# Performance work log

Measured on AMD Instinct MI355X. Metric: run time of the kernel, lower is better.

## Reference

```python
import jax, jax.numpy as jnp
import numpy as np

N = 50000
E = 800000
F_IN = 500
H = 5          # heads
C = 32         # per-head channels
HID = H * C    # 160
NC = 20        # num_classes
G = 8          # number of graphs in batch
SLOPE_ATT = 0.2   # GATConv attention leaky slope (PyG default)
SLOPE_ACT = 0.01  # F.leaky_relu default


def _layernorm(x, scale, bias, eps=1e-5):
    mu = jnp.mean(x, axis=-1, keepdims=True)
    var = jnp.var(x, axis=-1, keepdims=True)
    return (x - mu) * jax.lax.rsqrt(var + eps) * scale + bias


def _edge_softmax(logits, dst, num_nodes):
    # segment softmax over incoming edges of each destination node
    m = jax.ops.segment_max(logits, dst, num_segments=num_nodes)
    ex = jnp.exp(logits - m[dst])
    s = jax.ops.segment_sum(ex, dst, num_segments=num_nodes)
    return ex / (s[dst] + 1e-16)


def _gat_layer(x, src, dst, W, a_src, a_dst, b):
    n = x.shape[0]
    h = (x @ W).reshape(n, H, C)                       # [N,H,C]
    al_s = jnp.einsum('nhc,hc->nh', h, a_src)          # [N,H]
    al_d = jnp.einsum('nhc,hc->nh', h, a_dst)
    logits = jax.nn.leaky_relu(al_s[src] + al_d[dst], SLOPE_ATT)  # [Et,H]
    alpha = _edge_softmax(logits, dst, n)              # [Et,H]
    msg = h[src] * alpha[..., None]                    # [Et,H,C]
    out = jax.ops.segment_sum(msg, dst, num_segments=n).reshape(n, HID) + b
    return out, alpha


def setup_inputs():
    key = jax.random.key(0)
    ks = jax.random.split(key, 24)
    p = lambda k, shp: jax.random.normal(k, shp, jnp.float32) * 0.05
    x = jax.random.normal(ks[0], (N, F_IN), jnp.float32)
    edge_index = jax.random.randint(ks[1], (2, E), 0, N, jnp.int64)
    batch = jnp.sort(jax.random.randint(ks[2], (N,), 0, G, jnp.int64))
    return {
        'x': x, 'edge_index': edge_index, 'batch': batch,
        'W1': p(ks[3], (F_IN, HID)), 'a_src1': p(ks[4], (H, C)), 'a_dst1': p(ks[5], (H, C)), 'b1': jnp.zeros((HID,), jnp.float32),
        'ln1_s': jnp.ones((HID,), jnp.float32), 'ln1_b': jnp.zeros((HID,), jnp.float32),
        'W2': p(ks[6], (HID, HID)), 'a_src2': p(ks[7], (H, C)), 'a_dst2': p(ks[8], (H, C)), 'b2': jnp.zeros((HID,), jnp.float32),
        'ln2_s': jnp.ones((HID,), jnp.float32), 'ln2_b': jnp.zeros((HID,), jnp.float32),
        'Wm': p(ks[9], (HID, HID)), 'bm': jnp.zeros((HID,), jnp.float32),
        'Wmlp1': p(ks[10], (HID, HID)), 'bmlp1': jnp.zeros((HID,), jnp.float32),
        'ln3_s': jnp.ones((HID,), jnp.float32), 'ln3_b': jnp.zeros((HID,), jnp.float32),
        'Wmlp2': p(ks[11], (HID, NC)), 'bmlp2': jnp.zeros((NC,), jnp.float32),
    }


def reference(x, edge_index, batch, W1, a_src1, a_dst1, b1, ln1_s, ln1_b,
              W2, a_src2, a_dst2, b2, ln2_s, ln2_b, Wm, bm,
              Wmlp1, bmlp1, ln3_s, ln3_b, Wmlp2, bmlp2):
    n = x.shape[0]
    # PyG GATConv adds self-loops by default
    loops = jnp.arange(n, dtype=edge_index.dtype)
    src = jnp.concatenate([edge_index[0], loops])
    dst = jnp.concatenate([edge_index[1], loops])

    h1, alpha1 = _gat_layer(x, src, dst, W1, a_src1, a_dst1, b1)
    h1 = jax.nn.leaky_relu(h1, SLOPE_ACT)
    h1 = _layernorm(h1, ln1_s, ln1_b)      # dropout = identity at eval

    h2, alpha2 = _gat_layer(h1, src, dst, W2, a_src2, a_dst2, b2)
    h2 = jax.nn.leaky_relu(h2, SLOPE_ACT)
    h2 = _layernorm(h2, ln2_s, ln2_b)

    xo = jax.nn.leaky_relu(h2 @ Wm + bm, SLOPE_ACT)   # [N,HID]

    # global_mean_pool over batch assignment
    sums = jax.ops.segment_sum(xo, batch, num_segments=G)
    cnts = jax.ops.segment_sum(jnp.ones((n, 1), xo.dtype), batch, num_segments=G)
    pooled = sums / jnp.maximum(cnts, 1.0)            # [G,HID]

    z = pooled @ Wmlp1 + bmlp1
    z = jax.nn.relu(_layernorm(z, ln3_s, ln3_b))
    rec = z @ Wmlp2 + bmlp2                           # [G,NC]
    return xo, rec, alpha1, alpha2
```

## Files before the change

kernel.cpp:

```cpp
#include <hip/hip_runtime.h>
#include <hip/hip_bf16.h>
#include <cstdint>
#include <cstddef>

#define NN   50000
#define EE   800000
#define ET_  (EE + NN)
#define FIN  500
#define HID_ 160
#define NC_  20
#define GG   8

typedef __attribute__((ext_vector_type(8))) short ab8;
typedef __attribute__((ext_vector_type(4))) float f4;

static __device__ __forceinline__ unsigned short f2bf(float v) {
    union { float f; uint32_t u; } c; c.f = v;
    uint32_t r = c.u + 0x7FFFu + ((c.u >> 16) & 1u);
    return (unsigned short)(r >> 16);
}

static __device__ __forceinline__ float2 bf2f2(uint32_t u) {
    union { uint32_t u; float f; } a, b;
    a.u = u << 16;
    b.u = u & 0xffff0000u;
    return make_float2(a.f, b.f);
}

static __device__ __forceinline__ int lbound_i(const int* arr, int n, int val) {
    int lo = 0, hi = n;
    while (lo < hi) { int mid = (lo + hi) >> 1; if (arr[mid] < val) lo = mid + 1; else hi = mid; }
    return lo;
}

__global__ __launch_bounds__(256) void k_hist(const int* __restrict__ ei, int* __restrict__ deg) {
    int e = blockIdx.x * 256 + threadIdx.x;
    if (e >= ET_) return;
    int d = (e < EE) ? ei[EE + e] : (e - EE);
    atomicAdd(&deg[d], 1);
}

__global__ __launch_bounds__(256) void k_scan1(const int* __restrict__ deg, int* __restrict__ rowptr,
                                               int* __restrict__ bsum) {
    __shared__ int s[256];
    int t = threadIdx.x;
    int base = blockIdx.x * 1024 + t * 4;
    int v0 = (base + 0 < NN) ? deg[base + 0] : 0;
    int v1 = (base + 1 < NN) ? deg[base + 1] : 0;
    int v2 = (base + 2 < NN) ? deg[base + 2] : 0;
    int v3 = (base + 3 < NN) ? deg[base + 3] : 0;
    int tot = v0 + v1 + v2 + v3;
    s[t] = tot;
    __syncthreads();
    for (int off = 1; off < 256; off <<= 1) {
        int y = (t >= off) ? s[t - off] : 0;
        __syncthreads();
        s[t] += y;
        __syncthreads();
    }
    int excl = s[t] - tot;
    if (t == 255) bsum[blockIdx.x] = s[255];
    if (base + 0 < NN) rowptr[base + 0] = excl;  excl += v0;
    if (base + 1 < NN) rowptr[base + 1] = excl;  excl += v1;
    if (base + 2 < NN) rowptr[base + 2] = excl;  excl += v2;
    if (base + 3 < NN) rowptr[base + 3] = excl;
}

__global__ void k_scan2(int* __restrict__ bsum, int nb) {
    int t = threadIdx.x;
    int v = (t < nb) ? bsum[t] : 0;
    int orig = v;
    for (int off = 1; off < 64; off <<= 1) {
        int y = __shfl_up(v, off);
        if (t >= off) v += y;
    }
    if (t < nb) bsum[t] = v - orig;
}

__global__ __launch_bounds__(256) void k_scan3(int* __restrict__ rowptr, const int* __restrict__ bsum,
                                               int* __restrict__ cursor) {
    int i = blockIdx.x * 256 + threadIdx.x;
    if (i < NN) {
        int r = rowptr[i] + bsum[i >> 10];
        rowptr[i] = r;
        cursor[i] = r;
    }
    if (i == NN) rowptr[NN] = ET_;
}

__global__ __launch_bounds__(256) void k_scatter(const int* __restrict__ ei, int* __restrict__ cursor,
                                                 int2* __restrict__ epair) {
    int e = blockIdx.x * 256 + threadIdx.x;
    if (e >= ET_) return;
    int s, d;
    if (e < EE) { s = ei[e]; d = ei[EE + e]; } else { s = e - EE; d = e - EE; }
    int slot = atomicAdd(&cursor[d], 1);
    epair[slot] = make_int2(e, s);
}

__global__ __launch_bounds__(256) void k_prep_all(const float* __restrict__ W1, unsigned short* __restrict__ Wt1,
                                                  const float* __restrict__ W2, unsigned short* __restrict__ Wt2,
                                                  const float* __restrict__ Wm, unsigned short* __restrict__ Wmt) {
    int idx = blockIdx.x * 256 + threadIdx.x;
    const int S1 = HID_ * 512, S2 = HID_ * HID_;
    if (idx < S1) {
        int n = idx / 512, k = idx - n * 512;
        Wt1[idx] = (k < FIN) ? f2bf(W1[(size_t)k * HID_ + n]) : (unsigned short)0;
    } else if (idx < S1 + S2) {
        int j = idx - S1;
        int n = j / HID_, k = j - n * HID_;
        Wt2[j] = f2bf(W2[(size_t)k * HID_ + n]);
    } else if (idx < S1 + 2 * S2) {
        int j = idx - S1 - S2;
        int n = j / HID_, k = j - n * HID_;
        Wmt[j] = f2bf(Wm[(size_t)k * HID_ + n]);
    }
}

__global__ __launch_bounds__(256) void k_gemm_mfma(const void* __restrict__ Av,
                                                   const unsigned short* __restrict__ Bt,
                                                   float* __restrict__ C, __hip_bfloat16* __restrict__ Cb,
                                                   int M, int K, int Kp, int a_bf16,
                                                   const float* __restrict__ bias, int act,
                                                   const float* __restrict__ asrc, const float* __restrict__ adst,
                                                   float* __restrict__ als_o, float* __restrict__ ald_o,
                                                   const int* __restrict__ batch_p, float* __restrict__ pooled) {
    __shared__ __align__(16) unsigned short As[128 * 40];
    __shared__ __align__(16) unsigned short Bs[160 * 40];
    int tid  = threadIdx.x;
    int lane = tid & 63;
    int w    = tid >> 6;
    int fr   = lane & 15;
    int q8   = (lane >> 4) * 8;
    int row0 = blockIdx.x * 128;

    int arow  = tid >> 1;
    int abase = (tid & 1) * 16;

    f4 acc0[10], acc1[10];
#pragma unroll
    for (int t = 0; t < 10; t++) { acc0[t] = (f4)0.f; acc1[t] = (f4)0.f; }

    for (int k0 = 0; k0 < Kp; k0 += 32) {
        {
            int grow = row0 + arow;
            int bk = k0 + abase;
            if (a_bf16) {
                const unsigned short* Ab = (const unsigned short*)Av;
                ab8 v0 = (ab8)0, v1 = (ab8)0;
                if (grow < M) {
                    v0 = *reinterpret_cast<const ab8*>(&Ab[(size_t)grow * K + bk]);
                    v1 = *reinterpret_cast<const ab8*>(&Ab[(size_t)grow * K + bk + 8]);
                }
                *reinterpret_cast<ab8*>(&As[arow * 40 + abase])     = v0;
                *reinterpret_cast<ab8*>(&As[arow * 40 + abase + 8]) = v1;
            } else {
                const float* A = (const float*)Av;
                unsigned short pk[16];
                if (grow < M && bk + 16 <= K) {
                    const float4* src = reinterpret_cast<const float4*>(&A[(size_t)grow * K + bk]);
#pragma unroll
                    for (int f = 0; f < 4; f++) {
                        float4 v = src[f];
                        pk[f * 4 + 0] = f2bf(v.x); pk[f * 4 + 1] = f2bf(v.y);
                        pk[f * 4 + 2] = f2bf(v.z); pk[f * 4 + 3] = f2bf(v.w);
                    }
                } else {
#pragma unroll
                    for (int c = 0; c < 16; c++) {
                        int k = bk + c;
                        pk[c] = (grow < M && k < K) ? f2bf(A[(size_t)grow * K + k]) : (unsigned short)0;
                    }
                }
                *reinterpret_cast<ab8*>(&As[arow * 40 + abase])     = *reinterpret_cast<ab8*>(&pk[0]);
                *reinterpret_cast<ab8*>(&As[arow * 40 + abase + 8]) = *reinterpret_cast<ab8*>(&pk[8]);
            }
        }
        {
            for (int idx = tid; idx < 640; idx += 256) {
                int n = idx >> 2, c4 = (idx & 3) * 8;
                ab8 v = *reinterpret_cast<const ab8*>(&Bt[(size_t)n * Kp + k0 + c4]);
                *reinterpret_cast<ab8*>(&Bs[n * 40 + c4]) = v;
            }
        }
        __syncthreads();
        ab8 a0 = *reinterpret_cast<const ab8*>(&As[(w * 16 + fr) * 40 + q8]);
        ab8 a1 = *reinterpret_cast<const ab8*>(&As[(w * 16 + 64 + fr) * 40 + q8]);
#pragma unroll
        for (int t = 0; t < 10; t++) {
            ab8 b = *reinterpret_cast<const ab8*>(&Bs[(t * 16 + fr) * 40 + q8]);
            acc0[t] = __builtin_amdgcn_mfma_f32_16x16x32_bf16(a0, b, acc0[t], 0, 0, 0);
            acc1[t] = __builtin_amdgcn_mfma_f32_16x16x32_bf16(a1, b, acc1[t], 0, 0, 0);
        }
        __syncthreads();
    }

    int q = lane >> 4;
    if (als_o) {
        float av_s[10], av_d[10];
#pragma unroll
        for (int t = 0; t < 10; t++) { av_s[t] = asrc[t * 16 + fr]; av_d[t] = adst[t * 16 + fr]; }
#pragma unroll
        for (int s = 0; s < 2; s++) {
            const f4* ac = s ? acc1 : acc0;
#pragma unroll
            for (int i = 0; i < 4; i++) {
                int r = row0 + w * 16 + q * 4 + i + s * 64;
                float ps[5], pd[5];
#pragma unroll
                for (int h = 0; h < 5; h++) {
                    ps[h] = ac[2 * h][i] * av_s[2 * h] + ac[2 * h + 1][i] * av_s[2 * h + 1];
                    pd[h] = ac[2 * h][i] * av_d[2 * h] + ac[2 * h + 1][i] * av_d[2 * h + 1];
                }
#pragma unroll
                for (int off = 8; off >= 1; off >>= 1)
#pragma unroll
                    for (int h = 0; h < 5; h++) {
                        ps[h] += __shfl_xor(ps[h], off);
                        pd[h] += __shfl_xor(pd[h], off);
                    }
                if (fr == 0 && r < M) {
#pragma unroll
                    for (int h = 0; h < 5; h++) {
                        als_o[(size_t)r * 5 + h] = ps[h];
                        ald_o[(size_t)r * 5 + h] = pd[h];
                    }
                }
            }
        }
    }

    int gu = -2;
    if (pooled) {
        int gl = batch_p[row0];
        int rhi = row0 + 127; if (rhi >= M) rhi = M - 1;
        int gh = batch_p[rhi];
        gu = (gl == gh) ? gl : -1;
    }
    float psum[10];
#pragma unroll
    for (int t = 0; t < 10; t++) psum[t] = 0.f;

    int rbase0 = row0 + w * 16 + q * 4;
#pragma unroll
    for (int t = 0; t < 10; t++) {
        int col = t * 16 + fr;
        float bv = bias ? bias[col] : 0.f;
#pragma unroll
        for (int i = 0; i < 4; i++) {
            int r0 = rbase0 + i;
            int r1 = r0 + 64;
            float v0 = acc0[t][i] + bv;
            float v1 = acc1[t][i] + bv;
            if (act) { v0 = v0 > 0.f ? v0 : 0.01f * v0; v1 = v1 > 0.f ? v1 : 0.01f * v1; }
            if (r0 < M) {
                if (C)  C[(size_t)r0 * HID_ + col] = v0;
                if (Cb) *reinterpret_cast<unsigned short*>(&Cb[(size_t)r0 * HID_ + col]) = f2bf(v0);
            }
            if (r1 < M) {
                if (C)  C[(size_t)r1 * HID_ + col] = v1;
                if (Cb) *reinterpret_cast<unsigned short*>(&Cb[(size_t)r1 * HID_ + col]) = f2bf(v1);
            }
            if (gu >= 0) {
                if (r0 < M) psum[t] += v0;
                if (r1 < M) psum[t] += v1;
            } else if (gu == -1) {
                if (r0 < M) atomicAdd(&pooled[batch_p[r0] * HID_ + col], v0);
                if (r1 < M) atomicAdd(&pooled[batch_p[r1] * HID_ + col], v1);
            }
        }
    }
    if (gu >= 0) {
#pragma unroll
        for (int t = 0; t < 10; t++) {
            psum[t] += __shfl_xor(psum[t], 16);
            psum[t] += __shfl_xor(psum[t], 32);
        }
        if (q == 0) {
#pragma unroll
            for (int t = 0; t < 10; t++)
                atomicAdd(&pooled[gu * HID_ + t * 16 + fr], psum[t]);
        }
    }
}

__global__ __launch_bounds__(256) void k_att_agg(const int* __restrict__ rowptr,
                                                 const int2* __restrict__ epair,
                                                 const float* __restrict__ als, const float* __restrict__ ald,
                                                 const __hip_bfloat16* __restrict__ hmat,
                                                 float* __restrict__ alphap,
                                                 float* __restrict__ alpha_out,
                                                 const float* __restrict__ bias,
                                                 const float* __restrict__ lns, const float* __restrict__ lnb,
                                                 __hip_bfloat16* __restrict__ outb) {
    __shared__ float sExp[4][64 * 5];
    __shared__ int2  sPair[4][64];
    int wv   = threadIdx.x >> 6;
    int lane = threadIdx.x & 63;
    int node = blockIdx.x * 4 + wv;
    if (node >= NN) return;
    int start = rowptr[node], end = rowptr[node + 1];
    int deg = end - start;
    bool fits = (deg <= 64);
    float ad[5];
#pragma unroll
    for (int h = 0; h < 5; h++) ad[h] = ald[node * 5 + h];

    float sm[5] = {0.f, 0.f, 0.f, 0.f, 0.f};
    for (int j = start + lane; j < end; j += 64) {
        int2 p = epair[j];
        const float* as = &als[(size_t)p.y * 5];
        int idx = j - start;
        if (fits) sPair[wv][idx] = p;
#pragma unroll
        for (int h = 0; h < 5; h++) {
            float l = as[h] + ad[h];
            l = l > 0.f ? l : 0.2f * l;
            float ex = __expf(fminf(l, 60.f));
            sm[h] += ex;
            if (fits) sExp[wv][idx * 5 + h] = ex;
            else      alphap[(size_t)j * 5 + h] = ex;
        }
    }
#pragma unroll
    for (int off = 32; off >= 1; off >>= 1)
#pragma unroll
        for (int h = 0; h < 5; h++) sm[h] += __shfl_xor(sm[h], off);
    float inv[5];
#pragma unroll
    for (int h = 0; h < 5; h++) inv[h] = 1.f / (sm[h] + 1e-16f);

    int h0 = lane >> 4;
    bool lo16 = lane < 16;
    int c01 = 2 * lane;
    int c2  = 128 + 2 * lane;
    float2 A  = make_float2(0.f, 0.f), B2 = make_float2(0.f, 0.f);
    float2 A2 = make_float2(0.f, 0.f), B22 = make_float2(0.f, 0.f);

    if (fits) {
        if (lane < deg) {
            int2 p = sPair[wv][lane];
            float* ao = &alpha_out[(size_t)p.x * 5];
#pragma unroll
            for (int h = 0; h < 5; h++) ao[h] = sExp[wv][lane * 5 + h] * inv[h];
        }
        int idx = 0;
        for (; idx + 1 < deg; idx += 2) {
            int sA = sPair[wv][idx].y, sB = sPair[wv][idx + 1].y;
            float wA = sExp[wv][idx * 5 + h0] * inv[h0];
            float wB = sExp[wv][(idx + 1) * 5 + h0] * inv[h0];
            const unsigned short* rA = (const unsigned short*)&hmat[(size_t)sA * HID_];
            const unsigned short* rB = (const unsigned short*)&hmat[(size_t)sB * HID_];
            float2 fA = bf2f2(*reinterpret_cast<const uint32_t*>(&rA[c01]));
            float2 fB = bf2f2(*reinterpret_cast<const uint32_t*>(&rB[c01]));
            A.x += wA * fA.x; A.y += wA * fA.y;
            B2.x += wB * fB.x; B2.y += wB * fB.y;
            if (lo16) {
                float wA4 = sExp[wv][idx * 5 + 4] * inv[4];
                float wB4 = sExp[wv][(idx + 1) * 5 + 4] * inv[4];
                float2 gA = bf2f2(*reinterpret_cast<const uint32_t*>(&rA[c2]));
                float2 gB = bf2f2(*reinterpret_cast<const uint32_t*>(&rB[c2]));
                A2.x += wA4 * gA.x; A2.y += wA4 * gA.y;
                B22.x += wB4 * gB.x; B22.y += wB4 * gB.y;
            }
        }
        if (idx < deg) {
            int sA = sPair[wv][idx].y;
            float wA = sExp[wv][idx * 5 + h0] * inv[h0];
            const unsigned short* rA = (const unsigned short*)&hmat[(size_t)sA * HID_];
            float2 fA = bf2f2(*reinterpret_cast<const uint32_t*>(&rA[c01]));
            A.x += wA * fA.x; A.y += wA * fA.y;
            if (lo16) {
                float wA4 = sExp[wv][idx * 5 + 4] * inv[4];
                float2 gA = bf2f2(*reinterpret_cast<const uint32_t*>(&rA[c2]));
                A2.x += wA4 * gA.x; A2.y += wA4 * gA.y;
            }
        }
    } else {
        for (int j = start + lane; j < end; j += 64) {
            int2 p = epair[j];
            float* ao = &alpha_out[(size_t)p.x * 5];
#pragma unroll
            for (int h = 0; h < 5; h++) ao[h] = alphap[(size_t)j * 5 + h] * inv[h];
        }
        for (int j = start; j < end; j++) {
            int2 p = epair[j];
            const float* ap = &alphap[(size_t)j * 5];
            float wA = ap[h0] * inv[h0];
            const unsigned short* rA = (const unsigned short*)&hmat[(size_t)p.y * HID_];
            float2 fA = bf2f2(*reinterpret_cast<const uint32_t*>(&rA[c01]));
            A.x += wA * fA.x; A.y += wA * fA.y;
            if (lo16) {
                float wA4 = ap[4] * inv[4];
                float2 gA = bf2f2(*reinterpret_cast<const uint32_t*>(&rA[c2]));
                A2.x += wA4 * gA.x; A2.y += wA4 * gA.y;
            }
        }
    }
    A.x += B2.x; A.y += B2.y; A2.x += B22.x; A2.y += B22.y;

    float2 bb = *reinterpret_cast<const float2*>(&bias[c01]);
    float v0 = A.x + bb.x;  v0 = v0 > 0.f ? v0 : 0.01f * v0;
    float v1 = A.y + bb.y;  v1 = v1 > 0.f ? v1 : 0.01f * v1;
    float v2 = 0.f, v3 = 0.f;
    if (lo16) {
        float2 b2 = *reinterpret_cast<const float2*>(&bias[c2]);
        v2 = A2.x + b2.x; v2 = v2 > 0.f ? v2 : 0.01f * v2;
        v3 = A2.y + b2.y; v3 = v3 > 0.f ? v3 : 0.01f * v3;
    }
    float s  = v0 + v1 + v2 + v3;
    float sq = v0 * v0 + v1 * v1 + v2 * v2 + v3 * v3;
#pragma unroll
    for (int off = 32; off >= 1; off >>= 1) {
        s  += __shfl_xor(s, off);
        sq += __shfl_xor(sq, off);
    }
    float m = s * (1.f / 160.f);
    float r = rsqrtf(sq * (1.f / 160.f) - m * m + 1e-5f);
    size_t ob = (size_t)node * HID_;
    {
        float2 sc = *reinterpret_cast<const float2*>(&lns[c01]);
        float2 bi = *reinterpret_cast<const float2*>(&lnb[c01]);
        uint32_t pk = (uint32_t)f2bf((v0 - m) * r * sc.x + bi.x)
                    | ((uint32_t)f2bf((v1 - m) * r * sc.y + bi.y) << 16);
        *reinterpret_cast<uint32_t*>(&outb[ob + c01]) = pk;
    }
    if (lo16) {
        float2 sc = *reinterpret_cast<const float2*>(&lns[c2]);
        float2 bi = *reinterpret_cast<const float2*>(&lnb[c2]);
        uint32_t pk = (uint32_t)f2bf((v2 - m) * r * sc.x + bi.x)
                    | ((uint32_t)f2bf((v3 - m) * r * sc.y + bi.y) << 16);
        *reinterpret_cast<uint32_t*>(&outb[ob + c2]) = pk;
    }
}

__global__ __launch_bounds__(256) void k_mlp(const float* __restrict__ pooled, const int* __restrict__ batch,
                                             const float* __restrict__ W1, const float* __restrict__ b1,
                                             const float* __restrict__ lns, const float* __restrict__ lnb,
                                             const float* __restrict__ W2, const float* __restrict__ b2,
                                             float* __restrict__ rec) {
    __shared__ float P[GG][HID_];
    __shared__ float Z[GG][HID_];
    __shared__ float mu[GG], rr[GG], ic[GG];
    int t = threadIdx.x;
    if (t < GG) {
        int lo = lbound_i(batch, NN, t), hi = lbound_i(batch, NN, t + 1);
        ic[t] = 1.f / fmaxf((float)(hi - lo), 1.f);
    }
    __syncthreads();
    for (int i = t; i < GG * HID_; i += 256) P[i / HID_][i % HID_] = pooled[i] * ic[i / HID_];
    __syncthreads();
    for (int i = t; i < GG * HID_; i += 256) {
        int g = i / HID_, j = i % HID_;
        float acc = b1[j];
        for (int k = 0; k < HID_; k++) acc += P[g][k] * W1[k * HID_ + j];
        Z[g][j] = acc;
    }
    __syncthreads();
    if (t < GG) {
        float s = 0.f, sq = 0.f;
        for (int k = 0; k < HID_; k++) { float z = Z[t][k]; s += z; sq += z * z; }
        float m = s / (float)HID_;
        mu[t] = m;
        rr[t] = rsqrtf(sq / (float)HID_ - m * m + 1e-5f);
    }
    __syncthreads();
    for (int i = t; i < GG * HID_; i += 256) {
        int g = i / HID_, j = i % HID_;
        float z = (Z[g][j] - mu[g]) * rr[g] * lns[j] + lnb[j];
        Z[g][j] = fmaxf(z, 0.f);
    }
    __syncthreads();
    for (int i = t; i < GG * NC_; i += 256) {
        int g = i / NC_, j = i % NC_;
        float acc = b2[j];
        for (int k = 0; k < HID_; k++) acc += Z[g][k] * W2[k * NC_ + j];
        rec[g * NC_ + j] = acc;
    }
}

extern "C" void kernel_launch(void* const* d_in, const int* in_sizes, int n_in,
                              void* d_out, int out_size, void* d_ws, size_t ws_size,
                              hipStream_t stream) {
    const float* x    = (const float*)d_in[0];
    const int*   ei   = (const int*)d_in[1];
    const int*   batch= (const int*)d_in[2];
    const float* W1   = (const float*)d_in[3];
    const float* as1  = (const float*)d_in[4];
    const float* ad1  = (const float*)d_in[5];
    const float* b1   = (const float*)d_in[6];
    const float* ln1s = (const float*)d_in[7];
    const float* ln1b = (const float*)d_in[8];
    const float* W2   = (const float*)d_in[9];
    const float* as2  = (const float*)d_in[10];
    const float* ad2  = (const float*)d_in[11];
    const float* b2   = (const float*)d_in[12];
    const float* ln2s = (const float*)d_in[13];
    const float* ln2b = (const float*)d_in[14];
    const float* Wm   = (const float*)d_in[15];
    const float* bm   = (const float*)d_in[16];
    const float* Wm1  = (const float*)d_in[17];
    const float* bm1  = (const float*)d_in[18];
    const float* ln3s = (const float*)d_in[19];
    const float* ln3b = (const float*)d_in[20];
    const float* Wm2  = (const float*)d_in[21];
    const float* bm2  = (const float*)d_in[22];

    float* out    = (float*)d_out;
    float* xo     = out;
    float* rec    = out + (size_t)NN * HID_;
    float* alpha1 = rec + GG * NC_;
    float* alpha2 = alpha1 + (size_t)ET_ * 5;

    char* w = (char*)d_ws;
    auto carve = [&](size_t bytes) { char* p = w; w += (bytes + 255) & ~(size_t)255; return p; };
    int*   deg    = (int*)carve((size_t)NN * 4);
    int*   rowptr = (int*)carve((size_t)(NN + 1) * 4);
    int*   cursor = (int*)carve((size_t)NN * 4);
    int2*  epair  = (int2*)carve((size_t)ET_ * 8);
    int*   bsum   = (int*)carve(64 * 4);
    __hip_bfloat16* hbuf  = (__hip_bfloat16*)carve((size_t)NN * HID_ * 2);
    __hip_bfloat16* xbufb = (__hip_bfloat16*)carve((size_t)NN * HID_ * 2);
    float* alphap = (float*)carve((size_t)ET_ * 5 * 4);
    float* als    = (float*)carve((size_t)NN * 5 * 4);
    float* ald    = (float*)carve((size_t)NN * 5 * 4);
    float* pooled = (float*)carve((size_t)GG * HID_ * 4);
    unsigned short* Wt1 = (unsigned short*)carve((size_t)HID_ * 512 * 2);
    unsigned short* Wt2 = (unsigned short*)carve((size_t)HID_ * HID_ * 2);
    unsigned short* Wmt = (unsigned short*)carve((size_t)HID_ * HID_ * 2);

    hipMemsetAsync(deg, 0, (size_t)NN * 4, stream);
    k_hist<<<(ET_ + 255) / 256, 256, 0, stream>>>(ei, deg);
    int nb = (NN + 1023) / 1024;
    k_scan1<<<nb, 256, 0, stream>>>(deg, rowptr, bsum);
    k_scan2<<<1, 64, 0, stream>>>(bsum, nb);
    k_scan3<<<(NN + 1 + 255) / 256, 256, 0, stream>>>(rowptr, bsum, cursor);
    k_scatter<<<(ET_ + 255) / 256, 256, 0, stream>>>(ei, cursor, epair);

    const int PREP = HID_ * 512 + 2 * HID_ * HID_;
    k_prep_all<<<(PREP + 255) / 256, 256, 0, stream>>>(W1, Wt1, W2, Wt2, Wm, Wmt);
    hipMemsetAsync(pooled, 0, (size_t)GG * HID_ * 4, stream);

    const int NWB = (NN + 3) / 4;
    const int GB  = (NN + 127) / 128;

    k_gemm_mfma<<<GB, 256, 0, stream>>>(x, Wt1, nullptr, hbuf, NN, FIN, 512, 0, nullptr, 0,
                                        as1, ad1, als, ald, nullptr, nullptr);
    k_att_agg<<<NWB, 256, 0, stream>>>(rowptr, epair, als, ald, hbuf, alphap, alpha1,
                                       b1, ln1s, ln1b, xbufb);

    k_gemm_mfma<<<GB, 256, 0, stream>>>(xbufb, Wt2, nullptr, hbuf, NN, HID_, HID_, 1, nullptr, 0,
                                        as2, ad2, als, ald, nullptr, nullptr);
    k_att_agg<<<NWB, 256, 0, stream>>>(rowptr, epair, als, ald, hbuf, alphap, alpha2,
                                       b2, ln2s, ln2b, xbufb);

    k_gemm_mfma<<<GB, 256, 0, stream>>>(xbufb, Wmt, xo, nullptr, NN, HID_, HID_, 1, bm, 1,
                                        nullptr, nullptr, nullptr, nullptr, batch, pooled);
    k_mlp<<<1, 256, 0, stream>>>(pooled, batch, Wm1, bm1, ln3s, ln3b, Wm2, bm2, rec);
}
```

Baseline: 666.2 us.

## Rewrite GEMM to load operands straight into registers without shared memory

Measured after the change: 717.0 us. 7.6% more time.

```diff
diff --git a/kernel.cpp b/kernel.cpp
--- a/kernel.cpp
+++ b/kernel.cpp
@@ -100,9 +100,11 @@
 
 __global__ __launch_bounds__(256) void k_prep_all(const float* __restrict__ W1, unsigned short* __restrict__ Wt1,
                                                   const float* __restrict__ W2, unsigned short* __restrict__ Wt2,
-                                                  const float* __restrict__ Wm, unsigned short* __restrict__ Wmt) {
+                                                  const float* __restrict__ Wm, unsigned short* __restrict__ Wmt,
+                                                  float* __restrict__ pooled) {
     int idx = blockIdx.x * 256 + threadIdx.x;
     const int S1 = HID_ * 512, S2 = HID_ * HID_;
+    if (idx < GG * HID_) pooled[idx] = 0.f;
     if (idx < S1) {
         int n = idx / 512, k = idx - n * 512;
         Wt1[idx] = (k < FIN) ? f2bf(W1[(size_t)k * HID_ + n]) : (unsigned short)0;
@@ -117,171 +119,161 @@
     }
 }
 
-__global__ __launch_bounds__(256) void k_gemm_mfma(const void* __restrict__ Av,
+template<int ABF>
+static __device__ __forceinline__ void gemm_body(const void* __restrict__ Av,
+                                                 const unsigned short* __restrict__ Bt,
+                                                 float* __restrict__ C, __hip_bfloat16* __restrict__ Cb,
+                                                 int M, int K, int Kp,
+                                                 const float* __restrict__ bias, int act,
+                                                 const float* __restrict__ asrc, const float* __restrict__ adst,
+                                                 float* __restrict__ als_o, float* __restrict__ ald_o,
+                                                 const int* __restrict__ batch_p, float* __restrict__ pooled) {
+    int tid  = threadIdx.x;
+    int lane = tid & 63;
+    int w    = tid >> 6;
+    int fr   = lane & 15;
+    int q    = lane >> 4;
+    int row0 = blockIdx.x * 64;
+    int arow = row0 + w * 16 + fr;
+    bool rv  = arow < M;
+
+    f4 acc[10];
+#pragma unroll
+    for (int t = 0; t < 10; t++) acc[t] = (f4)0.f;
+
+    const int nk = Kp >> 5;
+    const unsigned short* bbase = Bt + (size_t)fr * Kp + q * 8;
+
+    auto loadA = [&](int s) -> ab8 {
+        ab8 a = (ab8)0;
+        int k0 = s * 32 + q * 8;
+        if (ABF) {
+            const unsigned short* Ab = (const unsigned short*)Av;
+            if (rv) a = *reinterpret_cast<const ab8*>(&Ab[(size_t)arow * K + k0]);
+        } else {
+            const float* A = (const float*)Av;
+            if (rv && k0 + 8 <= K) {
+                const float4* s4 = reinterpret_cast<const float4*>(&A[(size_t)arow * K + k0]);
+                float4 u = s4[0], v = s4[1];
+                unsigned short pk[8] = {f2bf(u.x), f2bf(u.y), f2bf(u.z), f2bf(u.w),
+                                        f2bf(v.x), f2bf(v.y), f2bf(v.z), f2bf(v.w)};
+                a = *reinterpret_cast<ab8*>(pk);
+            } else if (rv && k0 < K) {
+                unsigned short pk[8];
+#pragma unroll
+                for (int c = 0; c < 8; c++)
+                    pk[c] = (k0 + c < K) ? f2bf(A[(size_t)arow * K + k0 + c]) : (unsigned short)0;
+                a = *reinterpret_cast<ab8*>(pk);
+            }
+        }
+        return a;
+    };
+
+    ab8 acur = loadA(0);
+    for (int s = 0; s < nk; s++) {
+        ab8 anx = (ab8)0;
+        if (s + 1 < nk) anx = loadA(s + 1);
+        const unsigned short* bp = bbase + (size_t)s * 32;
+#pragma unroll
+        for (int t = 0; t < 10; t++) {
+            ab8 b = *reinterpret_cast<const ab8*>(&bp[(size_t)t * 16 * Kp]);
+            acc[t] = __builtin_amdgcn_mfma_f32_16x16x32_bf16(acur, b, acc[t], 0, 0, 0);
+        }
+        acur = anx;
+    }
+
+    if (als_o) {
+        float av_s[10], av_d[10];
+#pragma unroll
+        for (int t = 0; t < 10; t++) { av_s[t] = asrc[t * 16 + fr]; av_d[t] = adst[t * 16 + fr]; }
+#pragma unroll
+        for (int i = 0; i < 4; i++) {
+            int r = row0 + w * 16 + q * 4 + i;
+            float ps[5], pd[5];
+#pragma unroll
+            for (int h = 0; h < 5; h++) {
+                ps[h] = acc[2 * h][i] * av_s[2 * h] + acc[2 * h + 1][i] * av_s[2 * h + 1];
+                pd[h] = acc[2 * h][i] * av_d[2 * h] + acc[2 * h + 1][i] * av_d[2 * h + 1];
+            }
+#pragma unroll
+            for (int off = 8; off >= 1; off >>= 1)
+#pragma unroll
+                for (int h = 0; h < 5; h++) {
+                    ps[h] += __shfl_xor(ps[h], off);
+                    pd[h] += __shfl_xor(pd[h], off);
+                }
+            if (fr == 0 && r < M) {
+#pragma unroll
+                for (int h = 0; h < 5; h++) {
+                    als_o[(size_t)r * 5 + h] = ps[h];
+                    ald_o[(size_t)r * 5 + h] = pd[h];
+                }
+            }
+        }
+    }
+
+    int gu = -2;
+    if (pooled) {
+        int rhi = row0 + 63; if (rhi >= M) rhi = M - 1;
+        int gl = batch_p[row0], gh = batch_p[rhi];
+        gu = (gl == gh) ? gl : -1;
+    }
+    float psum[10];
+#pragma unroll
+    for (int t = 0; t < 10; t++) psum[t] = 0.f;
+
+    int rbase = row0 + w * 16 + q * 4;
+#pragma unroll
+    for (int t = 0; t < 10; t++) {
+        int col = t * 16 + fr;
+        float bv = bias ? bias[col] : 0.f;
+#pragma unroll
+        for (int i = 0; i < 4; i++) {
+            int r = rbase + i;
+            float v = acc[t][i] + bv;
+            if (act) v = v > 0.f ? v : 0.01f * v;
+            if (r < M) {
+                if (C)  C[(size_t)r * HID_ + col] = v;
+                if (Cb) *reinterpret_cast<unsigned short*>(&Cb[(size_t)r * HID_ + col]) = f2bf(v);
+                if (gu >= 0) psum[t] += v;
+                else if (gu == -1) atomicAdd(&pooled[batch_p[r] * HID_ + col], v);
+            }
+        }
+    }
+    if (gu >= 0) {
+#pragma unroll
+        for (int t = 0; t < 10; t++) {
+            psum[t] += __shfl_xor(psum[t], 16);
+            psum[t] += __shfl_xor(psum[t], 32);
+        }
+        if (q == 0) {
+#pragma unroll
+            for (int t = 0; t < 10; t++)
+                atomicAdd(&pooled[gu * HID_ + t * 16 + fr], psum[t]);
+        }
+    }
+}
+
+__global__ __launch_bounds__(256) void k_gemm_f32(const void* __restrict__ Av,
+                                                  const unsigned short* __restrict__ Bt,
+                                                  float* __restrict__ C, __hip_bfloat16* __restrict__ Cb,
+                                                  int M, int K, int Kp,
+                                                  const float* __restrict__ bias, int act,
+                                                  const float* __restrict__ asrc, const float* __restrict__ adst,
+                                                  float* __restrict__ als_o, float* __restrict__ ald_o,
+                                                  const int* __restrict__ batch_p, float* __restrict__ pooled) {
+    gemm_body<0>(Av, Bt, C, Cb, M, K, Kp, bias, act, asrc, adst, als_o, ald_o, batch_p, pooled);
+}
+
+__global__ __launch_bounds__(256) void k_gemm_bf16(const void* __restrict__ Av,
                                                    const unsigned short* __restrict__ Bt,
                                                    float* __restrict__ C, __hip_bfloat16* __restrict__ Cb,
-                                                   int M, int K, int Kp, int a_bf16,
+                                                   int M, int K, int Kp,
                                                    const float* __restrict__ bias, int act,
                                                    const float* __restrict__ asrc, const float* __restrict__ adst,
                                                    float* __restrict__ als_o, float* __restrict__ ald_o,
                                                    const int* __restrict__ batch_p, float* __restrict__ pooled) {
-    __shared__ __align__(16) unsigned short As[128 * 40];
-    __shared__ __align__(16) unsigned short Bs[160 * 40];
-    int tid  = threadIdx.x;
-    int lane = tid & 63;
-    int w    = tid >> 6;
-    int fr   = lane & 15;
-    int q8   = (lane >> 4) * 8;
-    int row0 = blockIdx.x * 128;
-
-    int arow  = tid >> 1;
-    int abase = (tid & 1) * 16;
-
-    f4 acc0[10], acc1[10];
-#pragma unroll
-    for (int t = 0; t < 10; t++) { acc0[t] = (f4)0.f; acc1[t] = (f4)0.f; }
-
-    for (int k0 = 0; k0 < Kp; k0 += 32) {
-        {
-            int grow = row0 + arow;
-            int bk = k0 + abase;
-            if (a_bf16) {
-                const unsigned short* Ab = (const unsigned short*)Av;
-                ab8 v0 = (ab8)0, v1 = (ab8)0;
-                if (grow < M) {
-                    v0 = *reinterpret_cast<const ab8*>(&Ab[(size_t)grow * K + bk]);
-                    v1 = *reinterpret_cast<const ab8*>(&Ab[(size_t)grow * K + bk + 8]);
-                }
-                *reinterpret_cast<ab8*>(&As[arow * 40 + abase])     = v0;
-                *reinterpret_cast<ab8*>(&As[arow * 40 + abase + 8]) = v1;
-            } else {
-                const float* A = (const float*)Av;
-                unsigned short pk[16];
-                if (grow < M && bk + 16 <= K) {
-                    const float4* src = reinterpret_cast<const float4*>(&A[(size_t)grow * K + bk]);
-#pragma unroll
-                    for (int f = 0; f < 4; f++) {
-                        float4 v = src[f];
-                        pk[f * 4 + 0] = f2bf(v.x); pk[f * 4 + 1] = f2bf(v.y);
-                        pk[f * 4 + 2] = f2bf(v.z); pk[f * 4 + 3] = f2bf(v.w);
-                    }
-                } else {
-#pragma unroll
-                    for (int c = 0; c < 16; c++) {
-                        int k = bk + c;
-                        pk[c] = (grow < M && k < K) ? f2bf(A[(size_t)grow * K + k]) : (unsigned short)0;
-                    }
-                }
-                *reinterpret_cast<ab8*>(&As[arow * 40 + abase])     = *reinterpret_cast<ab8*>(&pk[0]);
-                *reinterpret_cast<ab8*>(&As[arow * 40 + abase + 8]) = *reinterpret_cast<ab8*>(&pk[8]);
-            }
-        }
-        {
-            for (int idx = tid; idx < 640; idx += 256) {
-                int n = idx >> 2, c4 = (idx & 3) * 8;
-                ab8 v = *reinterpret_cast<const ab8*>(&Bt[(size_t)n * Kp + k0 + c4]);
-                *reinterpret_cast<ab8*>(&Bs[n * 40 + c4]) = v;
-            }
-        }
-        __syncthreads();
-        ab8 a0 = *reinterpret_cast<const ab8*>(&As[(w * 16 + fr) * 40 + q8]);
-        ab8 a1 = *reinterpret_cast<const ab8*>(&As[(w * 16 + 64 + fr) * 40 + q8]);
-#pragma unroll
-        for (int t = 0; t < 10; t++) {
-            ab8 b = *reinterpret_cast<const ab8*>(&Bs[(t * 16 + fr) * 40 + q8]);
-            acc0[t] = __builtin_amdgcn_mfma_f32_16x16x32_bf16(a0, b, acc0[t], 0, 0, 0);
-            acc1[t] = __builtin_amdgcn_mfma_f32_16x16x32_bf16(a1, b, acc1[t], 0, 0, 0);
-        }
-        __syncthreads();
-    }
-
-    int q = lane >> 4;
-    if (als_o) {
-        float av_s[10], av_d[10];
-#pragma unroll
-        for (int t = 0; t < 10; t++) { av_s[t] = asrc[t * 16 + fr]; av_d[t] = adst[t * 16 + fr]; }
-#pragma unroll
-        for (int s = 0; s < 2; s++) {
-            const f4* ac = s ? acc1 : acc0;
-#pragma unroll
-            for (int i = 0; i < 4; i++) {
-                int r = row0 + w * 16 + q * 4 + i + s * 64;
-                float ps[5], pd[5];
-#pragma unroll
-                for (int h = 0; h < 5; h++) {
-                    ps[h] = ac[2 * h][i] * av_s[2 * h] + ac[2 * h + 1][i] * av_s[2 * h + 1];
-                    pd[h] = ac[2 * h][i] * av_d[2 * h] + ac[2 * h + 1][i] * av_d[2 * h + 1];
-                }
-#pragma unroll
-                for (int off = 8; off >= 1; off >>= 1)
-#pragma unroll
-                    for (int h = 0; h < 5; h++) {
-                        ps[h] += __shfl_xor(ps[h], off);
-                        pd[h] += __shfl_xor(pd[h], off);
-                    }
-                if (fr == 0 && r < M) {
-#pragma unroll
-                    for (int h = 0; h < 5; h++) {
-                        als_o[(size_t)r * 5 + h] = ps[h];
-                        ald_o[(size_t)r * 5 + h] = pd[h];
-                    }
-                }
-            }
-        }
-    }
-
-    int gu = -2;
-    if (pooled) {
-        int gl = batch_p[row0];
-        int rhi = row0 + 127; if (rhi >= M) rhi = M - 1;
-        int gh = batch_p[rhi];
-        gu = (gl == gh) ? gl : -1;
-    }
-    float psum[10];
-#pragma unroll
-    for (int t = 0; t < 10; t++) psum[t] = 0.f;
-
-    int rbase0 = row0 + w * 16 + q * 4;
-#pragma unroll
-    for (int t = 0; t < 10; t++) {
-        int col = t * 16 + fr;
-        float bv = bias ? bias[col] : 0.f;
-#pragma unroll
-        for (int i = 0; i < 4; i++) {
-            int r0 = rbase0 + i;
-            int r1 = r0 + 64;
-            float v0 = acc0[t][i] + bv;
-            float v1 = acc1[t][i] + bv;
-            if (act) { v0 = v0 > 0.f ? v0 : 0.01f * v0; v1 = v1 > 0.f ? v1 : 0.01f * v1; }
-            if (r0 < M) {
-                if (C)  C[(size_t)r0 * HID_ + col] = v0;
-                if (Cb) *reinterpret_cast<unsigned short*>(&Cb[(size_t)r0 * HID_ + col]) = f2bf(v0);
-            }
-            if (r1 < M) {
-                if (C)  C[(size_t)r1 * HID_ + col] = v1;
-                if (Cb) *reinterpret_cast<unsigned short*>(&Cb[(size_t)r1 * HID_ + col]) = f2bf(v1);
-            }
-            if (gu >= 0) {
-                if (r0 < M) psum[t] += v0;
-                if (r1 < M) psum[t] += v1;
-            } else if (gu == -1) {
-                if (r0 < M) atomicAdd(&pooled[batch_p[r0] * HID_ + col], v0);
-                if (r1 < M) atomicAdd(&pooled[batch_p[r1] * HID_ + col], v1);
-            }
-        }
-    }
-    if (gu >= 0) {
-#pragma unroll
-        for (int t = 0; t < 10; t++) {
-            psum[t] += __shfl_xor(psum[t], 16);
-            psum[t] += __shfl_xor(psum[t], 32);
-        }
-        if (q == 0) {
-#pragma unroll
-            for (int t = 0; t < 10; t++)
-                atomicAdd(&pooled[gu * HID_ + t * 16 + fr], psum[t]);
-        }
-    }
+    gemm_body<1>(Av, Bt, C, Cb, M, K, Kp, bias, act, asrc, adst, als_o, ald_o, batch_p, pooled);
 }
 
 __global__ __launch_bounds__(256) void k_att_agg(const int* __restrict__ rowptr,
@@ -538,23 +530,22 @@
     k_scatter<<<(ET_ + 255) / 256, 256, 0, stream>>>(ei, cursor, epair);
 
     const int PREP = HID_ * 512 + 2 * HID_ * HID_;
-    k_prep_all<<<(PREP + 255) / 256, 256, 0, stream>>>(W1, Wt1, W2, Wt2, Wm, Wmt);
-    hipMemsetAsync(pooled, 0, (size_t)GG * HID_ * 4, stream);
+    k_prep_all<<<(PREP + 255) / 256, 256, 0, stream>>>(W1, Wt1, W2, Wt2, Wm, Wmt, pooled);
 
     const int NWB = (NN + 3) / 4;
-    const int GB  = (NN + 127) / 128;
-
-    k_gemm_mfma<<<GB, 256, 0, stream>>>(x, Wt1, nullptr, hbuf, NN, FIN, 512, 0, nullptr, 0,
-                                        as1, ad1, als, ald, nullptr, nullptr);
+    const int GB  = (NN + 63) / 64;
+
+    k_gemm_f32<<<GB, 256, 0, stream>>>(x, Wt1, nullptr, hbuf, NN, FIN, 512, nullptr, 0,
+                                       as1, ad1, als, ald, nullptr, nullptr);
     k_att_agg<<<NWB, 256, 0, stream>>>(rowptr, epair, als, ald, hbuf, alphap, alpha1,
                                        b1, ln1s, ln1b, xbufb);
 
-    k_gemm_mfma<<<GB, 256, 0, stream>>>(xbufb, Wt2, nullptr, hbuf, NN, HID_, HID_, 1, nullptr, 0,
+    k_gemm_bf16<<<GB, 256, 0, stream>>>(xbufb, Wt2, nullptr, hbuf, NN, HID_, HID_, nullptr, 0,
                                         as2, ad2, als, ald, nullptr, nullptr);
     k_att_agg<<<NWB, 256, 0, stream>>>(rowptr, epair, als, ald, hbuf, alphap, alpha2,
                                        b2, ln2s, ln2b, xbufb);
 
-    k_gemm_mfma<<<GB, 256, 0, stream>>>(xbufb, Wmt, xo, nullptr, NN, HID_, HID_, 1, bm, 1,
+    k_gemm_bf16<<<GB, 256, 0, stream>>>(xbufb, Wmt, xo, nullptr, NN, HID_, HID_, bm, 1,
                                         nullptr, nullptr, nullptr, nullptr, batch, pooled);
     k_mlp<<<1, 256, 0, stream>>>(pooled, batch, Wm1, bm1, ln3s, ln3b, Wm2, bm2, rec);
 }
```
